# Optimization experiments

Measured on AMD Instinct MI355X. Metric: run time of the kernel, lower is better.

Reference implementation:

```python
import jax, jax.numpy as jnp
import numpy as np

N_NODES = 50000
N_EDGES = 1600000
IN_CH = 512
HID_CH = 256


def _gcn_conv(x, edge_index, W, b):
    """PyG-style GCNConv: add self-loops, symmetric normalization, x@W then aggregate."""
    n = x.shape[0]
    loop = jnp.arange(n, dtype=edge_index.dtype)
    src = jnp.concatenate([edge_index[0], loop])  # [E+N]
    dst = jnp.concatenate([edge_index[1], loop])  # [E+N]
    deg = jax.ops.segment_sum(jnp.ones_like(dst, dtype=x.dtype), dst, num_segments=n)
    dinv = jnp.where(deg > 0, jax.lax.rsqrt(deg), 0.0)
    norm = dinv[src] * dinv[dst]  # [E+N]
    h = x @ W  # transform first (smaller feature dim for aggregation)
    msg = h[src] * norm[:, None]  # [E+N, F_out]
    out = jax.ops.segment_sum(msg, dst, num_segments=n)
    return out + b


def setup_inputs() -> dict:
    key = jax.random.key(0)
    ks = jax.random.split(key, 8)
    x = jax.random.normal(ks[0], (N_NODES, IN_CH), dtype=jnp.float32)
    edge_index = jax.random.randint(ks[1], (2, N_EDGES), 0, N_NODES, dtype=jnp.int32)
    W1 = jax.random.normal(ks[2], (IN_CH, HID_CH), dtype=jnp.float32) * (1.0 / np.sqrt(IN_CH))
    b1 = jnp.zeros((HID_CH,), dtype=jnp.float32)
    W2 = jax.random.normal(ks[3], (HID_CH, 32), dtype=jnp.float32) * (1.0 / np.sqrt(HID_CH))
    b2 = jnp.zeros((32,), dtype=jnp.float32)
    Wl = jax.random.normal(ks[4], (32, 2), dtype=jnp.float32) * (1.0 / np.sqrt(32))
    bl = jnp.zeros((2,), dtype=jnp.float32)
    return {"x": x, "edge_index": edge_index, "W1": W1, "b1": b1,
            "W2": W2, "b2": b2, "Wl": Wl, "bl": bl}


def reference(x, edge_index, W1, b1, W2, b2, Wl, bl):
    h = _gcn_conv(x, edge_index, W1, b1)
    h = jax.nn.relu(h)
    h = _gcn_conv(h, edge_index, W2, b2)
    # F.dropout(training=...) treated as identity (eval-mode reference)
    logits = h @ Wl + bl
    return jax.nn.log_softmax(logits, axis=1)
```

## Files before the change

### kernel.cpp

```cpp
#include <hip/hip_runtime.h>
#include <hip/hip_bf16.h>
#include <stdint.h>

#define NN 50000
#define NE 1600000
#define CIN 512
#define CH1 256
#define CH2 32

#define NBUCK 196
#define CAP 10240
#define CAP2 16384
#define ECH 4096
#define NCH 391

typedef __bf16 bf16_t;
typedef __attribute__((ext_vector_type(2))) __bf16 bf16x2;
typedef __attribute__((ext_vector_type(8))) __bf16 bf16x8;
typedef __attribute__((ext_vector_type(4))) float f32x4;
typedef __attribute__((ext_vector_type(2))) float f32x2;
typedef __attribute__((ext_vector_type(4))) uint32_t u32x4;

__device__ inline float blo(uint32_t v) { return __uint_as_float(v << 16); }
__device__ inline float bhi(uint32_t v) { return __uint_as_float(v & 0xffff0000u); }
__device__ inline uint32_t pk2(float a, float b) {
  bf16x2 p; p[0] = (__bf16)a; p[1] = (__bf16)b; return *(uint32_t*)&p;
}

__global__ __launch_bounds__(256) void k_hist(const int* __restrict__ dst,
                                              int* __restrict__ counts) {
  __shared__ int h[256];
  int blk = blockIdx.x, t = threadIdx.x;
  int e0 = blk * ECH;
  int ce = NE - e0; if (ce > ECH) ce = ECH;
  h[t] = 0;
  __syncthreads();
  for (int k = t; k < ce; k += 256) atomicAdd(&h[dst[e0 + k] >> 8], 1);
  __syncthreads();
  if (t < NBUCK) counts[blk * NBUCK + t] = h[t];
}

__global__ __launch_bounds__(512) void k_scanb(const int* __restrict__ counts,
                                               int* __restrict__ offs,
                                               int* __restrict__ bcnt) {
  __shared__ int l[512];
  int b = blockIdx.x, t = threadIdx.x;
  int v = (t < NCH) ? counts[t * NBUCK + b] : 0;
  int x = v;
  l[t] = x;
  __syncthreads();
  for (int off = 1; off < 512; off <<= 1) {
    int u = (t >= off) ? l[t - off] : 0;
    __syncthreads();
    x += u; l[t] = x;
    __syncthreads();
  }
  if (t < NCH) offs[t * NBUCK + b] = b * CAP + (x - v);
  if (t == 511) bcnt[b] = x;
}

__global__ __launch_bounds__(256) void k_bin(const int* __restrict__ src,
    const int* __restrict__ dst, const int* __restrict__ offs,
    uint32_t* __restrict__ binned) {
  __shared__ int lcnt[256], offsL[256];
  int blk = blockIdx.x, t = threadIdx.x;
  int e0 = blk * ECH;
  int ce = NE - e0; if (ce > ECH) ce = ECH;
  lcnt[t] = 0;
  if (t < NBUCK) offsL[t] = offs[blk * NBUCK + t];
  __syncthreads();
  for (int k = t; k < ce; k += 256) {
    int d = dst[e0 + k], s = src[e0 + k];
    int bkt = d >> 8;
    int p = atomicAdd(&lcnt[bkt], 1);
    binned[offsL[bkt] + p] = ((uint32_t)(d & 255) << 16) | (uint32_t)s;
  }
}

__global__ __launch_bounds__(256) void k_build(const uint32_t* __restrict__ binned,
    const int* __restrict__ bcnt, int* __restrict__ rowptr2, int* __restrict__ deg2,
    float* __restrict__ dinv, uint16_t* __restrict__ csrs) {
  __shared__ int hist[256], prow[256], lcnt[256];
  __shared__ int tot_s;
  __shared__ uint32_t c2[CAP2];
  int b = blockIdx.x, t = threadIdx.x;
  int count = bcnt[b];
  hist[t] = 0; lcnt[t] = 0;
  __syncthreads();
  const uint32_t* bb = binned + (size_t)b * CAP;
  for (int j = t; j < count; j += 256) atomicAdd(&hist[bb[j] >> 16], 1);
  __syncthreads();
  int node = b * 256 + t;
  int deg = hist[t];
  int pdeg = (node < NN) ? ((deg + 16) & ~15) : 0;
  int x = pdeg;
  prow[t] = x;
  __syncthreads();
  for (int off = 1; off < 256; off <<= 1) {
    int u = (t >= off) ? prow[t - off] : 0;
    __syncthreads();
    x += u; prow[t] = x;
    __syncthreads();
  }
  int start = x - pdeg;
  prow[t] = start;
  if (t == 255) tot_s = x;
  if (node < NN) {
    rowptr2[node] = b * CAP2 + start;
    deg2[node] = pdeg;
    dinv[node] = 1.0f / sqrtf((float)(deg + 1));
    c2[start + deg] = (uint32_t)node;
    for (int k = deg + 1; k < pdeg; ++k)
      c2[start + k] = (uint32_t)NN;
  }
  __syncthreads();
  for (int j = t; j < count; j += 256) {
    uint32_t e = bb[j];
    int dl = e >> 16;
    int p = prow[dl] + atomicAdd(&lcnt[dl], 1);
    c2[p] = e & 0xffffu;
  }
  __syncthreads();
  int tot = tot_s;
  uint16_t* co = csrs + (size_t)b * CAP2;
  for (int j = t; j < tot; j += 256) co[j] = (uint16_t)c2[j];
}

__global__ void k_prep_w(const float* __restrict__ W1, const float* __restrict__ W2,
                         bf16_t* __restrict__ w1t, bf16_t* __restrict__ w2t,
                         uint32_t* __restrict__ h1p_u32, uint32_t* __restrict__ h2b_u32) {
  int i = blockIdx.x * 256 + threadIdx.x;
  if (i < CIN * CH1) {
    int n = i >> 9, k = i & 511;
    w1t[i] = (__bf16)W1[k * CH1 + n];
  }
  if (i < CH1 * CH2) {
    int oc = i >> 8, k = i & 255;
    w2t[i] = (__bf16)W2[k * CH2 + oc];
  }
  if (blockIdx.x == 0) {
    int t = threadIdx.x;
    if (t < 128) {
      int p = t >> 4;
      h1p_u32[((size_t)p * (NN + 1) + NN) * 16 + (t & 15)] = 0;
    } else if (t < 144) {
      h2b_u32[(size_t)NN * 16 + (t - 128)] = 0;
    }
  }
}

#define BM 64
#define BN 256
#define BK 64

__global__ __launch_bounds__(256) void k_gemm1(const float* __restrict__ X,
                                               const bf16_t* __restrict__ BT,
                                               const float* __restrict__ dinv,
                                               bf16_t* __restrict__ h1p) {
  __shared__ __align__(16) bf16_t ldsA[2][BM * BK];
  __shared__ __align__(16) bf16_t ldsB[2][BN * BK];
  const int tid = threadIdx.x;
  const int lane = tid & 63;
  const int wid = tid >> 6;
  const int tm = blockIdx.x;

  f32x4 acc[4][4] = {};
  float4 ra[2], rb[2];

  auto loadA = [&](int kt) {
#pragma unroll
    for (int q = 0; q < 2; ++q) {
      int idx16 = q * 256 + tid;
      int r = idx16 >> 3, cw = idx16 & 7;
      int grow = tm * BM + r;
      grow = grow < NN ? grow : NN - 1;
      const float* ga = X + (size_t)grow * CIN + kt * BK + cw * 8;
      ra[q] = *(const float4*)ga;
      rb[q] = *(const float4*)(ga + 4);
    }
  };
  auto writeA = [&](int buf) {
#pragma unroll
    for (int q = 0; q < 2; ++q) {
      int idx16 = q * 256 + tid;
      int r = idx16 >> 3, cw = idx16 & 7;
      bf16x8 o;
      o[0] = (__bf16)ra[q].x; o[1] = (__bf16)ra[q].y;
      o[2] = (__bf16)ra[q].z; o[3] = (__bf16)ra[q].w;
      o[4] = (__bf16)rb[q].x; o[5] = (__bf16)rb[q].y;
      o[6] = (__bf16)rb[q].z; o[7] = (__bf16)rb[q].w;
      *(bf16x8*)&ldsA[buf][r * 64 + ((cw ^ (r & 7)) << 3)] = o;
    }
  };
  auto stageB = [&](int buf, int kt) {
#pragma unroll
    for (int t = 0; t < 8; ++t) {
      int o = t * 4096 + tid * 16;
      int r = o >> 7, cw = (o >> 4) & 7;
      int lc = cw ^ (r & 7);
      const bf16_t* gb = BT + (size_t)r * CIN + kt * BK + lc * 8;
      __builtin_amdgcn_global_load_lds(
          (const __attribute__((address_space(1))) void*)gb,
          (__attribute__((address_space(3))) void*)&ldsB[buf][(t * 4096 + wid * 1024) >> 1],
          16, 0, 0);
    }
  };

  loadA(0);
  stageB(0, 0);
  writeA(0);
  __syncthreads();
  int cur = 0;
  for (int kt = 0; kt < CIN / BK; ++kt) {
    if (kt + 1 < CIN / BK) { loadA(kt + 1); stageB(cur ^ 1, kt + 1); }
#pragma unroll
    for (int ks = 0; ks < 2; ++ks) {
      bf16x8 af[4], bfr[4];
#pragma unroll
      for (int m = 0; m < 4; ++m) {
        int row = m * 16 + (lane & 15);
        int kc = ks * 4 + (lane >> 4);
        af[m] = *(const bf16x8*)&ldsA[cur][row * 64 + ((kc ^ (row & 7)) << 3)];
      }
#pragma unroll
      for (int n = 0; n < 4; ++n) {
        int col = wid * 64 + n * 16 + (lane & 15);
        int kc = ks * 4 + (lane >> 4);
        bfr[n] = *(const bf16x8*)&ldsB[cur][col * 64 + ((kc ^ (col & 7)) << 3)];
      }
#pragma unroll
      for (int m = 0; m < 4; ++m)
#pragma unroll
        for (int n = 0; n < 4; ++n)
          acc[m][n] = __builtin_amdgcn_mfma_f32_16x16x32_bf16(af[m], bfr[n], acc[m][n], 0, 0, 0);
    }
    if (kt + 1 < CIN / BK) writeA(cur ^ 1);
    __syncthreads();
    cur ^= 1;
  }

#pragma unroll
  for (int m = 0; m < 4; ++m) {
#pragma unroll
    for (int r = 0; r < 4; ++r) {
      int grow = tm * BM + m * 16 + (lane >> 4) * 4 + r;
      if (grow < NN) {
        float dv = dinv[grow];
#pragma unroll
        for (int n = 0; n < 4; ++n) {
          int gcol = wid * 64 + n * 16 + (lane & 15);
          int plane = gcol >> 5, pc = gcol & 31;
          h1p[(size_t)plane * ((NN + 1) * 32) + (size_t)grow * 32 + pc] =
              (__bf16)(dv * acc[m][n][r]);
        }
      }
    }
  }
}

__global__ __launch_bounds__(256) void k_agg1(const uint32_t* __restrict__ h1p,
    const int* __restrict__ rowptr2, const int* __restrict__ deg2,
    const uint16_t* __restrict__ csrs, const float* __restrict__ dinv,
    const float* __restrict__ bias, uint32_t* __restrict__ hrp) {
  const int s = blockIdx.x & 7;
  const int lane = threadIdx.x & 63;
  const int wid = threadIdx.x >> 6;
  int i = (blockIdx.x >> 3) * 64 + wid * 16 + (lane >> 2);
  const bool valid = i < NN;
  i = valid ? i : NN - 1;
  const int cl = lane & 3;
  const int grp = lane & 60;
  const int cb = cl << 4;
  const char* __restrict__ Pb = (const char*)(h1p + (size_t)s * ((NN + 1) * 16));

  f32x2 a0 = {0.f, 0.f}, a1 = {0.f, 0.f}, a2 = {0.f, 0.f}, a3 = {0.f, 0.f};
  const int base = rowptr2[i];
  const int pdeg = deg2[i];
  uint32_t ent = __builtin_nontemporal_load((const uint32_t*)&csrs[base + cl * 2]);
  for (int b0 = 0; b0 < pdeg; b0 += 8) {
    uint32_t ent_n = __builtin_nontemporal_load(
        (const uint32_t*)&csrs[base + b0 + 8 + cl * 2]);
    int s0 = (int)(ent & 0xffffu) << 6;
    int s1 = (int)(ent >> 16) << 6;
#pragma unroll
    for (int e = 0; e < 8; ++e) {
      int off = __shfl((e & 1) ? s1 : s0, grp + (e >> 1)) + cb;
      u32x4 v = *(const u32x4*)(Pb + off);
      f32x2 f0 = {blo(v.x), bhi(v.x)};
      f32x2 f1 = {blo(v.y), bhi(v.y)};
      f32x2 f2 = {blo(v.z), bhi(v.z)};
      f32x2 f3 = {blo(v.w), bhi(v.w)};
      a0 += f0; a1 += f1; a2 += f2; a3 += f3;
    }
    ent = ent_n;
  }
  float di = dinv[i];
  float4 b0v = *(const float4*)&bias[s * 32 + cl * 8];
  float4 b1v = *(const float4*)&bias[s * 32 + cl * 8 + 4];
  u32x4 o;
  o.x = pk2(fmaxf(di * a0.x + b0v.x, 0.f), fmaxf(di * a0.y + b0v.y, 0.f));
  o.y = pk2(fmaxf(di * a1.x + b0v.z, 0.f), fmaxf(di * a1.y + b0v.w, 0.f));
  o.z = pk2(fmaxf(di * a2.x + b1v.x, 0.f), fmaxf(di * a2.y + b1v.y, 0.f));
  o.w = pk2(fmaxf(di * a3.x + b1v.z, 0.f), fmaxf(di * a3.y + b1v.w, 0.f));
  if (valid)
    __builtin_nontemporal_store(o,
        (u32x4*)&hrp[((size_t)s * NN + i) * 16 + cl * 4]);
}

__global__ __launch_bounds__(256) void k_gemm2(const bf16_t* __restrict__ hrp,
    const bf16_t* __restrict__ w2t, const float* __restrict__ dinv,
    bf16_t* __restrict__ h2b) {
  const int lane = threadIdx.x & 63;
  const int gw = blockIdx.x * 4 + (threadIdx.x >> 6);
  const int r0 = gw * 16;
  if (r0 >= NN) return;
  int arow = r0 + (lane & 15);
  arow = arow < NN ? arow : NN - 1;
  const int kc = lane >> 4;
  f32x4 acc0 = {}, acc1 = {};
#pragma unroll
  for (int kb = 0; kb < 8; ++kb) {
    bf16x8 a  = *(const bf16x8*)&hrp[(size_t)kb * (NN * 32) + (size_t)arow * 32 + kc * 8];
    bf16x8 b0 = *(const bf16x8*)&w2t[(size_t)(lane & 15) * CH1 + kb * 32 + kc * 8];
    bf16x8 b1 = *(const bf16x8*)&w2t[(size_t)(16 + (lane & 15)) * CH1 + kb * 32 + kc * 8];
    acc0 = __builtin_amdgcn_mfma_f32_16x16x32_bf16(a, b0, acc0, 0, 0, 0);
    acc1 = __builtin_amdgcn_mfma_f32_16x16x32_bf16(a, b1, acc1, 0, 0, 0);
  }
#pragma unroll
  for (int r = 0; r < 4; ++r) {
    int rr = r0 + (lane >> 4) * 4 + r;
    if (rr < NN) {
      float dv = dinv[rr];
      h2b[(size_t)rr * CH2 + (lane & 15)]      = (__bf16)(dv * acc0[r]);
      h2b[(size_t)rr * CH2 + 16 + (lane & 15)] = (__bf16)(dv * acc1[r]);
    }
  }
}

__global__ __launch_bounds__(256) void k_agg2(const uint32_t* __restrict__ h2b,
    const int* __restrict__ rowptr2, const int* __restrict__ deg2,
    const uint16_t* __restrict__ csrs, const float* __restrict__ dinv,
    const float* __restrict__ b2, const float* __restrict__ Wl,
    const float* __restrict__ bl, float* __restrict__ out) {
  const int lane = threadIdx.x & 63;
  const int wid = threadIdx.x >> 6;
  int i = blockIdx.x * 64 + wid * 16 + (lane >> 2);
  const bool valid = i < NN;
  i = valid ? i : NN - 1;
  const int cl = lane & 3;
  const int grp = lane & 60;
  const int cb = cl << 4;
  const char* __restrict__ Pb = (const char*)h2b;

  f32x2 a0 = {0.f, 0.f}, a1 = {0.f, 0.f}, a2 = {0.f, 0.f}, a3 = {0.f, 0.f};
  const int base = rowptr2[i];
  const int pdeg = deg2[i];
  uint32_t ent = __builtin_nontemporal_load((const uint32_t*)&csrs[base + cl * 2]);
  for (int b0 = 0; b0 < pdeg; b0 += 8) {
    uint32_t ent_n = __builtin_nontemporal_load(
        (const uint32_t*)&csrs[base + b0 + 8 + cl * 2]);
    int s0 = (int)(ent & 0xffffu) << 6;
    int s1 = (int)(ent >> 16) << 6;
#pragma unroll
    for (int e = 0; e < 8; ++e) {
      int off = __shfl((e & 1) ? s1 : s0, grp + (e >> 1)) + cb;
      u32x4 v = *(const u32x4*)(Pb + off);
      f32x2 f0 = {blo(v.x), bhi(v.x)};
      f32x2 f1 = {blo(v.y), bhi(v.y)};
      f32x2 f2 = {blo(v.z), bhi(v.z)};
      f32x2 f3 = {blo(v.w), bhi(v.w)};
      a0 += f0; a1 += f1; a2 += f2; a3 += f3;
    }
    ent = ent_n;
  }
  float di = dinv[i];
  float vv[8];
  vv[0] = di * a0.x + b2[cl * 8 + 0]; vv[1] = di * a0.y + b2[cl * 8 + 1];
  vv[2] = di * a1.x + b2[cl * 8 + 2]; vv[3] = di * a1.y + b2[cl * 8 + 3];
  vv[4] = di * a2.x + b2[cl * 8 + 4]; vv[5] = di * a2.y + b2[cl * 8 + 5];
  vv[6] = di * a3.x + b2[cl * 8 + 6]; vv[7] = di * a3.y + b2[cl * 8 + 7];
  float lp0 = 0.f, lp1 = 0.f;
  const float2* Wl2 = (const float2*)Wl;
#pragma unroll
  for (int k = 0; k < 8; ++k) {
    float2 wl = Wl2[cl * 8 + k];
    lp0 += vv[k] * wl.x;
    lp1 += vv[k] * wl.y;
  }
  lp0 += __shfl_xor(lp0, 1); lp0 += __shfl_xor(lp0, 2);
  lp1 += __shfl_xor(lp1, 1); lp1 += __shfl_xor(lp1, 2);
  if (valid && cl == 0) {
    float l0 = lp0 + bl[0], l1 = lp1 + bl[1];
    float m = fmaxf(l0, l1);
    float lse = m + logf(expf(l0 - m) + expf(l1 - m));
    float2 o; o.x = l0 - lse; o.y = l1 - lse;
    *(float2*)&out[i * 2] = o;
  }
}

extern "C" void kernel_launch(void* const* d_in, const int* in_sizes, int n_in,
                              void* d_out, int out_size, void* d_ws, size_t ws_size,
                              hipStream_t stream) {
  const float* x  = (const float*)d_in[0];
  const int*   ei = (const int*)d_in[1];
  const float* W1 = (const float*)d_in[2];
  const float* b1 = (const float*)d_in[3];
  const float* W2 = (const float*)d_in[4];
  const float* b2 = (const float*)d_in[5];
  const float* Wl = (const float*)d_in[6];
  const float* bl = (const float*)d_in[7];
  float* out = (float*)d_out;

  const int* src = ei;
  const int* dst = ei + NE;

  uint8_t* w = (uint8_t*)d_ws;
  auto alloc = [&](size_t bytes) { void* p = w; w += (bytes + 255) & ~(size_t)255; return p; };
  int*      counts = (int*)alloc((size_t)NCH * NBUCK * 4);
  int*      offs   = (int*)alloc((size_t)NCH * NBUCK * 4);
  int*      bcnt   = (int*)alloc((size_t)NBUCK * 4);
  uint32_t* binned = (uint32_t*)alloc((size_t)NBUCK * CAP * 4);
  uint16_t* csrs   = (uint16_t*)alloc((size_t)NBUCK * CAP2 * 2);
  int*      rowptr2= (int*)alloc((size_t)NN * 4);
  int*      deg2   = (int*)alloc((size_t)NN * 4);
  float*    dinv   = (float*)alloc((size_t)NN * 4);
  bf16_t*   w1t    = (bf16_t*)alloc((size_t)CIN * CH1 * 2);
  bf16_t*   w2t    = (bf16_t*)alloc((size_t)CH1 * CH2 * 2);
  bf16_t*   h1p    = (bf16_t*)alloc((size_t)(NN + 1) * CH1 * 2);
  bf16_t*   hrp    = (bf16_t*)alloc((size_t)NN * CH1 * 2);
  bf16_t*   h2b    = (bf16_t*)alloc((size_t)(NN + 1) * CH2 * 2);

  k_hist <<<NCH, 256, 0, stream>>>(dst, counts);
  k_scanb<<<NBUCK, 512, 0, stream>>>(counts, offs, bcnt);
  k_bin  <<<NCH, 256, 0, stream>>>(src, dst, offs, binned);
  k_build<<<NBUCK, 256, 0, stream>>>(binned, bcnt, rowptr2, deg2, dinv, csrs);

  k_prep_w<<<(CIN * CH1 + 255) / 256, 256, 0, stream>>>(W1, W2, w1t, w2t,
                                                        (uint32_t*)h1p, (uint32_t*)h2b);

  dim3 g1((NN + BM - 1) / BM);
  k_gemm1<<<g1, 256, 0, stream>>>(x, w1t, dinv, h1p);

  int nb = (NN + 63) / 64;
  k_agg1<<<nb * 8, 256, 0, stream>>>((const uint32_t*)h1p, rowptr2, deg2,
                                     csrs, dinv, b1, (uint32_t*)hrp);
  k_gemm2<<<(NN / 16 + 3) / 4, 256, 0, stream>>>(hrp, w2t, dinv, h2b);
  k_agg2<<<nb, 256, 0, stream>>>((const uint32_t*)h2b, rowptr2, deg2, csrs,
                                 dinv, b2, Wl, bl, out);
}
```

Measured before the change: 222.7 us.

## Split layer-1 aggregation into planar and contiguous-row gather paths

GEMM1 now also writes a second, row-contiguous copy of the transformed features. The layer-1 aggregation is split: the first 14016 nodes gather full 512-byte rows from that copy, 16 lanes per node, while the remaining nodes keep the 8-plane planar gather. The intent is to make each gather fetch a larger contiguous row and to balance the two access patterns. In exchange GEMM1 writes twice as much output, an extra 25 MB buffer is needed, and full rows have poorer cache locality per plane.

```diff
diff --git a/kernel.cpp b/kernel.cpp
--- a/kernel.cpp
+++ b/kernel.cpp
@@ -13,6 +13,10 @@
 #define CAP2 16384
 #define ECH 4096
 #define NCH 391
+
+#define NS  14016
+#define NBP ((NN - NS + 63) / 64)
+#define NBC (NS / 16)
 
 typedef __bf16 bf16_t;
 typedef __attribute__((ext_vector_type(2))) __bf16 bf16x2;
@@ -26,6 +30,11 @@
 __device__ inline uint32_t pk2(float a, float b) {
   bf16x2 p; p[0] = (__bf16)a; p[1] = (__bf16)b; return *(uint32_t*)&p;
 }
+#define RACC(v, A0, A1, A2, A3) { \
+    f32x2 t0 = {blo(v.x), bhi(v.x)}; A0 += t0; \
+    f32x2 t1 = {blo(v.y), bhi(v.y)}; A1 += t1; \
+    f32x2 t2 = {blo(v.z), bhi(v.z)}; A2 += t2; \
+    f32x2 t3 = {blo(v.w), bhi(v.w)}; A3 += t3; }
 
 __global__ __launch_bounds__(256) void k_hist(const int* __restrict__ dst,
                                               int* __restrict__ counts) {
@@ -128,7 +137,8 @@
 
 __global__ void k_prep_w(const float* __restrict__ W1, const float* __restrict__ W2,
                          bf16_t* __restrict__ w1t, bf16_t* __restrict__ w2t,
-                         uint32_t* __restrict__ h1p_u32, uint32_t* __restrict__ h2b_u32) {
+                         uint32_t* __restrict__ h1p_u32, uint32_t* __restrict__ h2b_u32,
+                         uint32_t* __restrict__ h1c_u32) {
   int i = blockIdx.x * 256 + threadIdx.x;
   if (i < CIN * CH1) {
     int n = i >> 9, k = i & 511;
@@ -146,6 +156,9 @@
     } else if (t < 144) {
       h2b_u32[(size_t)NN * 16 + (t - 128)] = 0;
     }
+  } else if (blockIdx.x == 1) {
+    int t = threadIdx.x;
+    if (t < 128) h1c_u32[(size_t)NN * 128 + t] = 0;
   }
 }
 
@@ -156,7 +169,8 @@
 __global__ __launch_bounds__(256) void k_gemm1(const float* __restrict__ X,
                                                const bf16_t* __restrict__ BT,
                                                const float* __restrict__ dinv,
-                                               bf16_t* __restrict__ h1p) {
+                                               bf16_t* __restrict__ h1p,
+                                               bf16_t* __restrict__ h1c) {
   __shared__ __align__(16) bf16_t ldsA[2][BM * BK];
   __shared__ __align__(16) bf16_t ldsB[2][BN * BK];
   const int tid = threadIdx.x;
@@ -250,8 +264,9 @@
         for (int n = 0; n < 4; ++n) {
           int gcol = wid * 64 + n * 16 + (lane & 15);
           int plane = gcol >> 5, pc = gcol & 31;
-          h1p[(size_t)plane * ((NN + 1) * 32) + (size_t)grow * 32 + pc] =
-              (__bf16)(dv * acc[m][n][r]);
+          bf16_t val = (__bf16)(dv * acc[m][n][r]);
+          h1p[(size_t)plane * ((NN + 1) * 32) + (size_t)grow * 32 + pc] = val;
+          h1c[(size_t)grow * 256 + gcol] = val;
         }
       }
     }
@@ -259,52 +274,95 @@
 }
 
 __global__ __launch_bounds__(256) void k_agg1(const uint32_t* __restrict__ h1p,
+    const uint32_t* __restrict__ h1c,
     const int* __restrict__ rowptr2, const int* __restrict__ deg2,
     const uint16_t* __restrict__ csrs, const float* __restrict__ dinv,
     const float* __restrict__ bias, uint32_t* __restrict__ hrp) {
-  const int s = blockIdx.x & 7;
   const int lane = threadIdx.x & 63;
   const int wid = threadIdx.x >> 6;
-  int i = (blockIdx.x >> 3) * 64 + wid * 16 + (lane >> 2);
-  const bool valid = i < NN;
-  i = valid ? i : NN - 1;
-  const int cl = lane & 3;
-  const int grp = lane & 60;
-  const int cb = cl << 4;
-  const char* __restrict__ Pb = (const char*)(h1p + (size_t)s * ((NN + 1) * 16));
-
-  f32x2 a0 = {0.f, 0.f}, a1 = {0.f, 0.f}, a2 = {0.f, 0.f}, a3 = {0.f, 0.f};
-  const int base = rowptr2[i];
-  const int pdeg = deg2[i];
-  uint32_t ent = __builtin_nontemporal_load((const uint32_t*)&csrs[base + cl * 2]);
-  for (int b0 = 0; b0 < pdeg; b0 += 8) {
-    uint32_t ent_n = __builtin_nontemporal_load(
-        (const uint32_t*)&csrs[base + b0 + 8 + cl * 2]);
-    int s0 = (int)(ent & 0xffffu) << 6;
-    int s1 = (int)(ent >> 16) << 6;
-#pragma unroll
-    for (int e = 0; e < 8; ++e) {
-      int off = __shfl((e & 1) ? s1 : s0, grp + (e >> 1)) + cb;
-      u32x4 v = *(const u32x4*)(Pb + off);
-      f32x2 f0 = {blo(v.x), bhi(v.x)};
-      f32x2 f1 = {blo(v.y), bhi(v.y)};
-      f32x2 f2 = {blo(v.z), bhi(v.z)};
-      f32x2 f3 = {blo(v.w), bhi(v.w)};
-      a0 += f0; a1 += f1; a2 += f2; a3 += f3;
-    }
-    ent = ent_n;
-  }
-  float di = dinv[i];
-  float4 b0v = *(const float4*)&bias[s * 32 + cl * 8];
-  float4 b1v = *(const float4*)&bias[s * 32 + cl * 8 + 4];
-  u32x4 o;
-  o.x = pk2(fmaxf(di * a0.x + b0v.x, 0.f), fmaxf(di * a0.y + b0v.y, 0.f));
-  o.y = pk2(fmaxf(di * a1.x + b0v.z, 0.f), fmaxf(di * a1.y + b0v.w, 0.f));
-  o.z = pk2(fmaxf(di * a2.x + b1v.x, 0.f), fmaxf(di * a2.y + b1v.y, 0.f));
-  o.w = pk2(fmaxf(di * a3.x + b1v.z, 0.f), fmaxf(di * a3.y + b1v.w, 0.f));
-  if (valid)
-    __builtin_nontemporal_store(o,
-        (u32x4*)&hrp[((size_t)s * NN + i) * 16 + cl * 4]);
+  if (blockIdx.x < NBP * 8) {
+    const int s = blockIdx.x & 7;
+    int i = NS + (blockIdx.x >> 3) * 64 + wid * 16 + (lane >> 2);
+    const bool valid = i < NN;
+    i = valid ? i : NN - 1;
+    const int cl = lane & 3;
+    const int grp = lane & 60;
+    const int cb = cl << 4;
+    const char* __restrict__ Pb = (const char*)(h1p + (size_t)s * ((NN + 1) * 16));
+
+    f32x2 a0 = {0.f, 0.f}, a1 = {0.f, 0.f}, a2 = {0.f, 0.f}, a3 = {0.f, 0.f};
+    const int base = rowptr2[i];
+    const int pdeg = deg2[i];
+    uint32_t ent = __builtin_nontemporal_load((const uint32_t*)&csrs[base + cl * 2]);
+    for (int b0 = 0; b0 < pdeg; b0 += 8) {
+      uint32_t ent_n = __builtin_nontemporal_load(
+          (const uint32_t*)&csrs[base + b0 + 8 + cl * 2]);
+      int s0 = (int)(ent & 0xffffu) << 6;
+      int s1 = (int)(ent >> 16) << 6;
+#pragma unroll
+      for (int e = 0; e < 8; ++e) {
+        int off = __shfl((e & 1) ? s1 : s0, grp + (e >> 1)) + cb;
+        u32x4 v = *(const u32x4*)(Pb + off);
+        RACC(v, a0, a1, a2, a3);
+      }
+      ent = ent_n;
+    }
+    float di = dinv[i];
+    float4 b0v = *(const float4*)&bias[s * 32 + cl * 8];
+    float4 b1v = *(const float4*)&bias[s * 32 + cl * 8 + 4];
+    u32x4 o;
+    o.x = pk2(fmaxf(di * a0.x + b0v.x, 0.f), fmaxf(di * a0.y + b0v.y, 0.f));
+    o.y = pk2(fmaxf(di * a1.x + b0v.z, 0.f), fmaxf(di * a1.y + b0v.w, 0.f));
+    o.z = pk2(fmaxf(di * a2.x + b1v.x, 0.f), fmaxf(di * a2.y + b1v.y, 0.f));
+    o.w = pk2(fmaxf(di * a3.x + b1v.z, 0.f), fmaxf(di * a3.y + b1v.w, 0.f));
+    if (valid)
+      __builtin_nontemporal_store(o,
+          (u32x4*)&hrp[((size_t)s * NN + i) * 16 + cl * 4]);
+  } else {
+    const int bidx = blockIdx.x - NBP * 8;
+    const int i = bidx * 16 + wid * 4 + (lane >> 4);
+    const int cl = lane & 15;
+    const int grp = lane & 48;
+    const int cb = cl << 5;
+    const char* __restrict__ Pb = (const char*)h1c;
+
+    f32x2 a0 = {0.f, 0.f}, a1 = {0.f, 0.f}, a2 = {0.f, 0.f}, a3 = {0.f, 0.f};
+    f32x2 a4 = {0.f, 0.f}, a5 = {0.f, 0.f}, a6 = {0.f, 0.f}, a7 = {0.f, 0.f};
+    const int base = rowptr2[i];
+    const int pdeg = deg2[i];
+    int ent = (int)__builtin_nontemporal_load(&csrs[base + cl]);
+    for (int b0 = 0; b0 < pdeg; b0 += 16) {
+      int ent_n = (int)__builtin_nontemporal_load(&csrs[base + b0 + 16 + cl]);
+      int sc = ent << 9;
+#pragma unroll
+      for (int e = 0; e < 16; ++e) {
+        int off = __shfl(sc, grp + e) + cb;
+        u32x4 v = __builtin_nontemporal_load((const u32x4*)(Pb + off));
+        u32x4 w = __builtin_nontemporal_load((const u32x4*)(Pb + off + 16));
+        RACC(v, a0, a1, a2, a3);
+        RACC(w, a4, a5, a6, a7);
+      }
+      ent = ent_n;
+    }
+    float di = dinv[i];
+    float4 q0 = *(const float4*)&bias[cl * 16 + 0];
+    float4 q1 = *(const float4*)&bias[cl * 16 + 4];
+    float4 q2 = *(const float4*)&bias[cl * 16 + 8];
+    float4 q3 = *(const float4*)&bias[cl * 16 + 12];
+    u32x4 o0, o1;
+    o0.x = pk2(fmaxf(di * a0.x + q0.x, 0.f), fmaxf(di * a0.y + q0.y, 0.f));
+    o0.y = pk2(fmaxf(di * a1.x + q0.z, 0.f), fmaxf(di * a1.y + q0.w, 0.f));
+    o0.z = pk2(fmaxf(di * a2.x + q1.x, 0.f), fmaxf(di * a2.y + q1.y, 0.f));
+    o0.w = pk2(fmaxf(di * a3.x + q1.z, 0.f), fmaxf(di * a3.y + q1.w, 0.f));
+    o1.x = pk2(fmaxf(di * a4.x + q2.x, 0.f), fmaxf(di * a4.y + q2.y, 0.f));
+    o1.y = pk2(fmaxf(di * a5.x + q2.z, 0.f), fmaxf(di * a5.y + q2.w, 0.f));
+    o1.z = pk2(fmaxf(di * a6.x + q3.x, 0.f), fmaxf(di * a6.y + q3.y, 0.f));
+    o1.w = pk2(fmaxf(di * a7.x + q3.z, 0.f), fmaxf(di * a7.y + q3.w, 0.f));
+    const int kb = cl >> 1;
+    size_t idx = ((size_t)kb * NN + i) * 16 + (cl & 1) * 8;
+    __builtin_nontemporal_store(o0, (u32x4*)&hrp[idx]);
+    __builtin_nontemporal_store(o1, (u32x4*)&hrp[idx + 4]);
+  }
 }
 
 __global__ __launch_bounds__(256) void k_gemm2(const bf16_t* __restrict__ hrp,
@@ -365,11 +423,7 @@
     for (int e = 0; e < 8; ++e) {
       int off = __shfl((e & 1) ? s1 : s0, grp + (e >> 1)) + cb;
       u32x4 v = *(const u32x4*)(Pb + off);
-      f32x2 f0 = {blo(v.x), bhi(v.x)};
-      f32x2 f1 = {blo(v.y), bhi(v.y)};
-      f32x2 f2 = {blo(v.z), bhi(v.z)};
-      f32x2 f3 = {blo(v.w), bhi(v.w)};
-      a0 += f0; a1 += f1; a2 += f2; a3 += f3;
+      RACC(v, a0, a1, a2, a3);
     }
     ent = ent_n;
   }
@@ -427,6 +481,7 @@
   bf16_t*   w1t    = (bf16_t*)alloc((size_t)CIN * CH1 * 2);
   bf16_t*   w2t    = (bf16_t*)alloc((size_t)CH1 * CH2 * 2);
   bf16_t*   h1p    = (bf16_t*)alloc((size_t)(NN + 1) * CH1 * 2);
+  bf16_t*   h1c    = (bf16_t*)alloc((size_t)(NN + 1) * CH1 * 2);
   bf16_t*   hrp    = (bf16_t*)alloc((size_t)NN * CH1 * 2);
   bf16_t*   h2b    = (bf16_t*)alloc((size_t)(NN + 1) * CH2 * 2);
 
@@ -436,15 +491,15 @@
   k_build<<<NBUCK, 256, 0, stream>>>(binned, bcnt, rowptr2, deg2, dinv, csrs);
 
   k_prep_w<<<(CIN * CH1 + 255) / 256, 256, 0, stream>>>(W1, W2, w1t, w2t,
-                                                        (uint32_t*)h1p, (uint32_t*)h2b);
+      (uint32_t*)h1p, (uint32_t*)h2b, (uint32_t*)h1c);
 
   dim3 g1((NN + BM - 1) / BM);
-  k_gemm1<<<g1, 256, 0, stream>>>(x, w1t, dinv, h1p);
-
+  k_gemm1<<<g1, 256, 0, stream>>>(x, w1t, dinv, h1p, h1c);
+
+  k_agg1<<<NBP * 8 + NBC, 256, 0, stream>>>((const uint32_t*)h1p,
+      (const uint32_t*)h1c, rowptr2, deg2, csrs, dinv, b1, (uint32_t*)hrp);
+  k_gemm2<<<(NN / 16 + 3) / 4, 256, 0, stream>>>(hrp, w2t, dinv, h2b);
   int nb = (NN + 63) / 64;
-  k_agg1<<<nb * 8, 256, 0, stream>>>((const uint32_t*)h1p, rowptr2, deg2,
-                                     csrs, dinv, b1, (uint32_t*)hrp);
-  k_gemm2<<<(NN / 16 + 3) / 4, 256, 0, stream>>>(hrp, w2t, dinv, h2b);
   k_agg2<<<nb, 256, 0, stream>>>((const uint32_t*)h2b, rowptr2, deg2, csrs,
                                  dinv, b2, Wl, bl, out);
 }
```

Result: slower. 263.5 us (+18.3%).
